# Performance work log

Measured on AMD Instinct MI355X. Metric: run time of the kernel, lower is better.

The kernel has to match this reference:

```python
import jax, jax.numpy as jnp
import numpy as np

EMBED = 1024
HEADS = 16
HEAD_DIM = EMBED // HEADS
SCALING = HEAD_DIM ** -0.5
R = 16
LORA_SCALE = 32.0 / R  # alpha / r
NEG = jnp.finfo(jnp.float32).min


def lora_linear(x, W, A, B):
    # y = x @ W.T + (x @ A.T) @ B.T * scale   (LinearLora, bias=False)
    return x @ W.T + ((x @ A.T) @ B.T) * LORA_SCALE


def setup_inputs() -> dict:
    key = jax.random.key(0)
    ks = jax.random.split(key, 14)
    B, T, D = 1, 4096, EMBED
    hidden_states = jax.random.normal(ks[0], (B, T, D), jnp.float32)
    # causal additive mask (bsz, 1, tgt, src): 0 on/below diag, dtype-min above
    i = jnp.arange(T)
    causal = jnp.where(i[:, None] >= i[None, :], 0.0, NEG).astype(jnp.float32)
    attention_mask = jnp.broadcast_to(causal, (B, 1, T, T))
    s = 0.02
    def w(k, shape):
        return jax.random.normal(k, shape, jnp.float32) * s
    return dict(
        hidden_states=hidden_states,
        attention_mask=attention_mask,
        Wq=w(ks[1], (D, D)), Wk=w(ks[2], (D, D)), Wv=w(ks[3], (D, D)), Wo=w(ks[4], (D, D)),
        Aq=w(ks[5], (R, D)), Bq=jnp.zeros((D, R), jnp.float32) + w(ks[6], (D, R)),
        Ak=w(ks[7], (R, D)), Bk=w(ks[8], (D, R)),
        Av=w(ks[9], (R, D)), Bv=w(ks[10], (D, R)),
        Ao=w(ks[11], (R, D)), Bo=w(ks[12], (D, R)),
    )


def reference(hidden_states, attention_mask, Wq, Wk, Wv, Wo,
              Aq, Bq, Ak, Bk, Av, Bv, Ao, Bo):
    bsz, tgt_len, _ = hidden_states.shape
    H, Hd = HEADS, HEAD_DIM

    q = lora_linear(hidden_states, Wq, Aq, Bq) * SCALING
    k = lora_linear(hidden_states, Wk, Ak, Bk)
    v = lora_linear(hidden_states, Wv, Av, Bv)

    # (b, t, H, Hd)
    q = q.reshape(bsz, tgt_len, H, Hd)
    k = k.reshape(bsz, tgt_len, H, Hd)
    v = v.reshape(bsz, tgt_len, H, Hd)

    # scores (b, H, t, s)
    attn = jnp.einsum('bthd,bshd->bhts', q, k)
    attn = attn + attention_mask
    attn = jnp.maximum(attn, NEG)
    attn = jax.nn.softmax(attn, axis=-1)  # dropout p=0 / eval mode

    out = jnp.einsum('bhts,bshd->bthd', attn, v)
    out = out.reshape(bsz, tgt_len, H * Hd)
    out = lora_linear(out, Wo, Ao, Bo)
    return out
```

## Files before the change

kernel.cpp:

```cpp
#include <hip/hip_runtime.h>
#include <cmath>
#include <cstdint>

typedef unsigned short u16;
typedef __attribute__((ext_vector_type(8))) __bf16 bf16x8;
typedef __attribute__((ext_vector_type(4))) __bf16 bf16x4;
typedef __attribute__((ext_vector_type(4))) short s16x4;
typedef __attribute__((ext_vector_type(4))) float f32x4;

__device__ __forceinline__ u16 f2bf(float f) {
    union { float f; unsigned u; } v; v.f = f;
    unsigned r = v.u + 0x7fffu + ((v.u >> 16) & 1u);
    return (u16)(r >> 16);
}

__device__ __forceinline__ void gload_lds(const u16* g, u16* l) {
    __builtin_amdgcn_global_load_lds((__attribute__((address_space(1))) void*)g,
                                     (__attribute__((address_space(3))) void*)l,
                                     16, 0, 0);
}

__device__ __forceinline__ f32x4 mfma16(s16x4 a, s16x4 b, f32x4 c) {
#if __has_builtin(__builtin_amdgcn_mfma_f32_16x16x16bf16_1k)
    return __builtin_amdgcn_mfma_f32_16x16x16bf16_1k(a, b, c, 0, 0, 0);
#else
    asm("v_mfma_f32_16x16x16_bf16 %0, %1, %2, %3"
        : "=v"(c) : "v"(a), "v"(b), "0"(c));
    return c;
#endif
}

__global__ __launch_bounds__(256) void prep_all(
        const float* __restrict__ X,
        const float* __restrict__ Wq, const float* __restrict__ Wk,
        const float* __restrict__ Wv, const float* __restrict__ Wo,
        const float* __restrict__ Aq, const float* __restrict__ Bq,
        const float* __restrict__ Ak, const float* __restrict__ Bk,
        const float* __restrict__ Av, const float* __restrict__ Bv,
        const float* __restrict__ Ao, const float* __restrict__ Bo,
        u16* __restrict__ Wqkv, u16* __restrict__ Wob, u16* __restrict__ Xb) {
    const int p = blockIdx.y;
    const int idx = blockIdx.x * 256 + threadIdx.x;
    if (p == 4) {
        float4 v = ((const float4*)X)[idx];
        ushort4 o;
        o.x = f2bf(v.x); o.y = f2bf(v.y); o.z = f2bf(v.z); o.w = f2bf(v.w);
        ((ushort4*)Xb)[idx] = o;
        return;
    }
    const int n = idx >> 10, d = idx & 1023;
    const float* W; const float* A; const float* B;
    switch (p) {
        case 0: W = Wq; A = Aq; B = Bq; break;
        case 1: W = Wk; A = Ak; B = Bk; break;
        case 2: W = Wv; A = Av; B = Bv; break;
        default: W = Wo; A = Ao; B = Bo; break;
    }
    float lora = 0.f;
#pragma unroll
    for (int r = 0; r < 16; r++) lora += B[n * 16 + r] * A[r * 1024 + d];
    float v = W[idx] + 2.0f * lora;
    if (p == 0) v *= 0.125f * 1.44269504088896340736f;
    if (p < 3) Wqkv[(size_t)p * 1048576 + idx] = f2bf(v);
    else       Wob[idx] = f2bf(v);
}

template <bool F32OUT>
__global__ __launch_bounds__(256, 3) void gemm_bt(const u16* __restrict__ A,
                                                  const u16* __restrict__ B,
                                                  void* __restrict__ C, int ldc) {
    __shared__ __align__(16) u16 As[128 * 64];
    __shared__ __align__(16) u16 Bs[128 * 64];
    const int tid = threadIdx.x;
    const int lane = tid & 63, wave = tid >> 6;
    const int quad = lane >> 4, l16 = lane & 15;
    const int wm = (wave >> 1) * 64, wn = (wave & 1) * 64;
    const size_t m0 = (size_t)blockIdx.y * 128, n0 = (size_t)blockIdx.x * 128;
    const u16* Ap = A + m0 * 1024;
    const u16* Bp = B + n0 * 1024;
    const int xsw = l16 & 7;
    f32x4 acc[4][4] = {};
    for (int k0 = 0; k0 < 1024; k0 += 64) {
#pragma unroll
        for (int hh = 0; hh < 4; hh++) {
            int c = tid + hh * 256;
            int row = c >> 3, cg = (c & 7) ^ (row & 7);
            gload_lds(Ap + (size_t)row * 1024 + k0 + cg * 8, As + c * 8);
            gload_lds(Bp + (size_t)row * 1024 + k0 + cg * 8, Bs + c * 8);
        }
        asm volatile("s_waitcnt vmcnt(0)" ::: "memory");
        __syncthreads();
#pragma unroll
        for (int kf = 0; kf < 2; kf++) {
            bf16x8 af[4], bfr[4];
#pragma unroll
            for (int i = 0; i < 4; i++) {
                af[i]  = *(const bf16x8*)(As + (wm + i * 16 + l16) * 64
                                             + ((kf * 4 + quad) ^ xsw) * 8);
                bfr[i] = *(const bf16x8*)(Bs + (wn + i * 16 + l16) * 64
                                             + ((kf * 4 + quad) ^ xsw) * 8);
            }
#pragma unroll
            for (int mi = 0; mi < 4; mi++)
#pragma unroll
                for (int ni = 0; ni < 4; ni++)
                    acc[mi][ni] = __builtin_amdgcn_mfma_f32_16x16x32_bf16(
                            af[mi], bfr[ni], acc[mi][ni], 0, 0, 0);
        }
        __syncthreads();
    }
#pragma unroll
    for (int mi = 0; mi < 4; mi++)
#pragma unroll
        for (int ni = 0; ni < 4; ni++)
#pragma unroll
            for (int r = 0; r < 4; r++) {
                size_t row = m0 + wm + mi * 16 + quad * 4 + r;
                size_t col = n0 + wn + ni * 16 + l16;
                if (F32OUT) ((float*)C)[row * ldc + col] = acc[mi][ni][r];
                else        ((u16*)C)[row * ldc + col] = f2bf(acc[mi][ni][r]);
            }
}

template <bool F32OUT>
__global__ __launch_bounds__(256, 3) void gemm_bt64(const u16* __restrict__ A,
                                                    const u16* __restrict__ B,
                                                    void* __restrict__ C, int ldc) {
    __shared__ __align__(16) u16 As[64 * 64];
    __shared__ __align__(16) u16 Bs[128 * 64];
    const int tid = threadIdx.x;
    const int lane = tid & 63, wave = tid >> 6;
    const int quad = lane >> 4, l16 = lane & 15;
    const int wm = (wave >> 1) * 32, wn = (wave & 1) * 64;
    const size_t m0 = (size_t)blockIdx.y * 64, n0 = (size_t)blockIdx.x * 128;
    const u16* Ap = A + m0 * 1024;
    const u16* Bp = B + n0 * 1024;
    const int xsw = l16 & 7;
    f32x4 acc[2][4] = {};
    for (int k0 = 0; k0 < 1024; k0 += 64) {
#pragma unroll
        for (int hh = 0; hh < 2; hh++) {
            int c = tid + hh * 256;
            int row = c >> 3, cg = (c & 7) ^ (row & 7);
            gload_lds(Ap + (size_t)row * 1024 + k0 + cg * 8, As + c * 8);
        }
#pragma unroll
        for (int hh = 0; hh < 4; hh++) {
            int c = tid + hh * 256;
            int row = c >> 3, cg = (c & 7) ^ (row & 7);
            gload_lds(Bp + (size_t)row * 1024 + k0 + cg * 8, Bs + c * 8);
        }
        asm volatile("s_waitcnt vmcnt(0)" ::: "memory");
        __syncthreads();
#pragma unroll
        for (int kf = 0; kf < 2; kf++) {
            bf16x8 af[2], bfr[4];
#pragma unroll
            for (int i = 0; i < 2; i++)
                af[i] = *(const bf16x8*)(As + (wm + i * 16 + l16) * 64
                                            + ((kf * 4 + quad) ^ xsw) * 8);
#pragma unroll
            for (int i = 0; i < 4; i++)
                bfr[i] = *(const bf16x8*)(Bs + (wn + i * 16 + l16) * 64
                                             + ((kf * 4 + quad) ^ xsw) * 8);
#pragma unroll
            for (int mi = 0; mi < 2; mi++)
#pragma unroll
                for (int ni = 0; ni < 4; ni++)
                    acc[mi][ni] = __builtin_amdgcn_mfma_f32_16x16x32_bf16(
                            af[mi], bfr[ni], acc[mi][ni], 0, 0, 0);
        }
        __syncthreads();
    }
#pragma unroll
    for (int mi = 0; mi < 2; mi++)
#pragma unroll
        for (int ni = 0; ni < 4; ni++)
#pragma unroll
            for (int r = 0; r < 4; r++) {
                size_t row = m0 + wm + mi * 16 + quad * 4 + r;
                size_t col = n0 + wn + ni * 16 + l16;
                if (F32OUT) ((float*)C)[row * ldc + col] = acc[mi][ni][r];
                else        ((u16*)C)[row * ldc + col] = f2bf(acc[mi][ni][r]);
            }
}

__global__ __launch_bounds__(256) void transpose_v(const u16* __restrict__ Y,
                                                   u16* __restrict__ Vt) {
    __shared__ u16 tile[64][68];
    const int dv0 = blockIdx.x * 64;
    const int t0  = blockIdx.y * 64;
    const int tid = threadIdx.x;
#pragma unroll
    for (int p = 0; p < 4; p++) {
        int pos = tid + p * 256;
        int row = pos >> 4;
        int c4  = (pos & 15) * 4;
        ushort4 v = *(const ushort4*)(Y + (size_t)(t0 + row) * 3072 + 2048 + dv0 + c4);
        tile[row][c4 + 0] = v.x; tile[row][c4 + 1] = v.y;
        tile[row][c4 + 2] = v.z; tile[row][c4 + 3] = v.w;
    }
    __syncthreads();
#pragma unroll
    for (int p = 0; p < 4; p++) {
        int pos = tid + p * 256;
        int orow = pos >> 4;
        int oc4  = (pos & 15) * 4;
        ushort4 o;
        o.x = tile[oc4 + 0][orow]; o.y = tile[oc4 + 1][orow];
        o.z = tile[oc4 + 2][orow]; o.w = tile[oc4 + 3][orow];
        *(ushort4*)(Vt + (size_t)(dv0 + orow) * 4096 + t0 + oc4) = o;
    }
}

__global__ __launch_bounds__(256, 4) void flash_attn(const u16* __restrict__ Y,
                                                     const u16* __restrict__ Vt,
                                                     u16* __restrict__ O) {
    __shared__ __align__(16) u16 lds[16384];
    const int tid = threadIdx.x;
    const int wave = tid >> 6, lane = tid & 63;
    const int quad = lane >> 4, l16 = lane & 15;
    const int bid = blockIdx.x;
    const int rr = bid & 255, j = bid >> 8;
    const int b = rr >> 4, h = rr & 15;
    int p;
    switch (j) { case 0:  p = 63 - b; break;
                 case 1:  p = 32 + b; break;
                 case 2:  p = 31 - b; break;
                 default: p = b;      break; }
    const int q0 = p * 64;
    const int q0w = q0 + wave * 16;
    const int nT = p + 1;
    const u16* Kbase = Y + 1024 + h * 64;
    const u16* Vbase = Vt + (size_t)(h * 64) * 4096;
    const int xsw = l16 & 7;

    bf16x8 qf[2];
#pragma unroll
    for (int kf = 0; kf < 2; kf++)
        qf[kf] = *(const bf16x8*)(Y + (size_t)(q0w + l16) * 3072
                                    + h * 64 + kf * 32 + quad * 8);

    f32x4 oaccT[4] = {};
    float l_i = 0.f;

#pragma unroll
    for (int pp = 0; pp < 2; pp++) {
        int c = pp * 256 + tid;
        int row = c >> 3, cg = (c & 7) ^ (row & 7);
        gload_lds(Kbase + (size_t)row * 3072 + cg * 8, lds + c * 8);
        gload_lds(Vbase + (size_t)row * 4096 + cg * 8, lds + 4096 + c * 8);
    }

#pragma unroll 1
    for (int t = 0; t < nT; t++) {
        const int s0 = t * 64;
        u16* Ks = lds + (t & 1) * 8192;
        u16* Vs = Ks + 4096;
        asm volatile("s_waitcnt vmcnt(0)" ::: "memory");
        __syncthreads();

        if (t + 1 < nT) {
            u16* Kn = lds + ((t + 1) & 1) * 8192;
            const int sn = s0 + 64;
#pragma unroll
            for (int pp = 0; pp < 2; pp++) {
                int c = pp * 256 + tid;
                int row = c >> 3, cg = (c & 7) ^ (row & 7);
                gload_lds(Kbase + (size_t)(sn + row) * 3072 + cg * 8, Kn + c * 8);
                gload_lds(Vbase + (size_t)row * 4096 + sn + cg * 8, Kn + 4096 + c * 8);
            }
        }

        bf16x8 kfr[4][2];
#pragma unroll
        for (int ni = 0; ni < 4; ni++) {
            int row = ni * 16 + l16;
            kfr[ni][0] = *(const bf16x8*)(Ks + row * 64 + ((quad) ^ xsw) * 8);
            kfr[ni][1] = *(const bf16x8*)(Ks + row * 64 + ((4 + quad) ^ xsw) * 8);
        }
        s16x4 vfr[4][4];
#pragma unroll
        for (int nj = 0; nj < 4; nj++) {
            int row = nj * 16 + l16;
#pragma unroll
            for (int ni = 0; ni < 4; ni++) {
                int cc = ni * 2 + (quad >> 1);
                vfr[nj][ni] = *(const s16x4*)(Vs + row * 64 + (cc ^ xsw) * 8
                                                 + (quad & 1) * 4);
            }
        }
        asm volatile("s_waitcnt lgkmcnt(0)" ::: "memory");

        f32x4 sacc[4] = {};
#pragma unroll
        for (int ni = 0; ni < 4; ni++) {
            sacc[ni] = __builtin_amdgcn_mfma_f32_16x16x32_bf16(
                    kfr[ni][0], qf[0], sacc[ni], 0, 0, 0);
            sacc[ni] = __builtin_amdgcn_mfma_f32_16x16x32_bf16(
                    kfr[ni][1], qf[1], sacc[ni], 0, 0, 0);
        }

        if (t == nT - 1) {
            const int qg = q0w + l16;
#pragma unroll
            for (int ni = 0; ni < 4; ni++)
#pragma unroll
                for (int r = 0; r < 4; r++) {
                    int sg = s0 + ni * 16 + quad * 4 + r;
                    if (sg > qg) sacc[ni][r] = -INFINITY;
                }
        }
        float rs = 0.f;
        s16x4 pf[4];
#pragma unroll
        for (int ni = 0; ni < 4; ni++) {
            f32x4 pe;
#pragma unroll
            for (int r = 0; r < 4; r++) {
                pe[r] = __builtin_amdgcn_exp2f(sacc[ni][r]);
                rs += pe[r];
            }
            bf16x4 tt = { (__bf16)pe[0], (__bf16)pe[1],
                          (__bf16)pe[2], (__bf16)pe[3] };
            pf[ni] = __builtin_bit_cast(s16x4, tt);
        }
        rs += __shfl_xor(rs, 16);
        rs += __shfl_xor(rs, 32);
        l_i += rs;

#pragma unroll
        for (int nj = 0; nj < 4; nj++)
#pragma unroll
            for (int ni = 0; ni < 4; ni++)
                oaccT[nj] = mfma16(vfr[nj][ni], pf[ni], oaccT[nj]);
    }

    __syncthreads();
    u16* scr = lds + wave * 1152;
    {
        float inv = 1.0f / l_i;
#pragma unroll
        for (int nj = 0; nj < 4; nj++) {
            bf16x4 t4 = { (__bf16)(oaccT[nj][0] * inv),
                          (__bf16)(oaccT[nj][1] * inv),
                          (__bf16)(oaccT[nj][2] * inv),
                          (__bf16)(oaccT[nj][3] * inv) };
            *(s16x4*)(scr + l16 * 72 + nj * 16 + quad * 4) =
                    __builtin_bit_cast(s16x4, t4);
        }
    }
    asm volatile("s_waitcnt lgkmcnt(0)" ::: "memory");
#pragma unroll
    for (int pp = 0; pp < 2; pp++) {
        int row = pp * 8 + (lane >> 3);
        int seg = (lane & 7) * 8;
        bf16x8 d = *(const bf16x8*)(scr + row * 72 + seg);
        *(bf16x8*)(O + (size_t)(q0w + row) * 1024 + h * 64 + seg) = d;
    }
}


extern "C" void kernel_launch(void* const* d_in, const int* in_sizes, int n_in,
                              void* d_out, int out_size, void* d_ws, size_t ws_size,
                              hipStream_t stream) {
    const float* X  = (const float*)d_in[0];
    const float* Wq = (const float*)d_in[2];
    const float* Wk = (const float*)d_in[3];
    const float* Wv = (const float*)d_in[4];
    const float* Wo = (const float*)d_in[5];
    const float* Aq = (const float*)d_in[6];
    const float* Bq = (const float*)d_in[7];
    const float* Ak = (const float*)d_in[8];
    const float* Bk = (const float*)d_in[9];
    const float* Av = (const float*)d_in[10];
    const float* Bv = (const float*)d_in[11];
    const float* Ao = (const float*)d_in[12];
    const float* Bo = (const float*)d_in[13];

    char* ws = (char*)d_ws;
    u16* Xb   = (u16*)(ws);
    u16* Wqkv = (u16*)(ws + (8u  << 20));
    u16* Wob  = (u16*)(ws + (14u << 20));
    u16* Y    = (u16*)(ws + (16u << 20));
    u16* Vt   = (u16*)(ws + (40u << 20));
    u16* Ob   = (u16*)(ws + (48u << 20));

    prep_all<<<dim3(4096, 5), 256, 0, stream>>>(X, Wq, Wk, Wv, Wo, Aq, Bq, Ak, Bk,
                                                Av, Bv, Ao, Bo, Wqkv, Wob, Xb);
    gemm_bt<false><<<dim3(24, 32), 256, 0, stream>>>(Xb, Wqkv, Y, 3072);
    transpose_v<<<dim3(16, 64), 256, 0, stream>>>(Y, Vt);
    flash_attn<<<dim3(1024), 256, 0, stream>>>(Y, Vt, Ob);
    gemm_bt64<true><<<dim3(8, 64), 256, 0, stream>>>(Ob, Wob, d_out, 1024);
}
```

Measured before the change: 257.3 us.

## Fuse V transpose into QKV GEMM epilogue and widen flash-attention query tiles

```diff
diff --git a/kernel.cpp b/kernel.cpp
--- a/kernel.cpp
+++ b/kernel.cpp
@@ -65,10 +65,10 @@
     else       Wob[idx] = f2bf(v);
 }
 
-template <bool F32OUT>
-__global__ __launch_bounds__(256, 3) void gemm_bt(const u16* __restrict__ A,
-                                                  const u16* __restrict__ B,
-                                                  void* __restrict__ C, int ldc) {
+__global__ __launch_bounds__(256, 3) void gemm_qkv(const u16* __restrict__ A,
+                                                   const u16* __restrict__ B,
+                                                   u16* __restrict__ Y,
+                                                   u16* __restrict__ Vt) {
     __shared__ __align__(16) u16 As[128 * 64];
     __shared__ __align__(16) u16 Bs[128 * 64];
     const int tid = threadIdx.x;
@@ -109,23 +109,35 @@
         }
         __syncthreads();
     }
-#pragma unroll
-    for (int mi = 0; mi < 4; mi++)
-#pragma unroll
-        for (int ni = 0; ni < 4; ni++)
-#pragma unroll
-            for (int r = 0; r < 4; r++) {
-                size_t row = m0 + wm + mi * 16 + quad * 4 + r;
-                size_t col = n0 + wn + ni * 16 + l16;
-                if (F32OUT) ((float*)C)[row * ldc + col] = acc[mi][ni][r];
-                else        ((u16*)C)[row * ldc + col] = f2bf(acc[mi][ni][r]);
-            }
-}
-
-template <bool F32OUT>
+    if (n0 >= 2048) {
+#pragma unroll
+        for (int mi = 0; mi < 4; mi++)
+#pragma unroll
+            for (int ni = 0; ni < 4; ni++) {
+                size_t dv = n0 - 2048 + wn + ni * 16 + l16;
+                size_t t  = m0 + wm + mi * 16 + quad * 4;
+                ushort4 pk;
+                pk.x = f2bf(acc[mi][ni][0]); pk.y = f2bf(acc[mi][ni][1]);
+                pk.z = f2bf(acc[mi][ni][2]); pk.w = f2bf(acc[mi][ni][3]);
+                *(ushort4*)(Vt + dv * 4096 + t) = pk;
+            }
+    } else {
+#pragma unroll
+        for (int mi = 0; mi < 4; mi++)
+#pragma unroll
+            for (int ni = 0; ni < 4; ni++)
+#pragma unroll
+                for (int r = 0; r < 4; r++) {
+                    size_t row = m0 + wm + mi * 16 + quad * 4 + r;
+                    size_t col = n0 + wn + ni * 16 + l16;
+                    Y[row * 2048 + col] = f2bf(acc[mi][ni][r]);
+                }
+    }
+}
+
 __global__ __launch_bounds__(256, 3) void gemm_bt64(const u16* __restrict__ A,
                                                     const u16* __restrict__ B,
-                                                    void* __restrict__ C, int ldc) {
+                                                    float* __restrict__ C) {
     __shared__ __align__(16) u16 As[64 * 64];
     __shared__ __align__(16) u16 Bs[128 * 64];
     const int tid = threadIdx.x;
@@ -180,75 +192,43 @@
             for (int r = 0; r < 4; r++) {
                 size_t row = m0 + wm + mi * 16 + quad * 4 + r;
                 size_t col = n0 + wn + ni * 16 + l16;
-                if (F32OUT) ((float*)C)[row * ldc + col] = acc[mi][ni][r];
-                else        ((u16*)C)[row * ldc + col] = f2bf(acc[mi][ni][r]);
-            }
-}
-
-__global__ __launch_bounds__(256) void transpose_v(const u16* __restrict__ Y,
-                                                   u16* __restrict__ Vt) {
-    __shared__ u16 tile[64][68];
-    const int dv0 = blockIdx.x * 64;
-    const int t0  = blockIdx.y * 64;
-    const int tid = threadIdx.x;
-#pragma unroll
-    for (int p = 0; p < 4; p++) {
-        int pos = tid + p * 256;
-        int row = pos >> 4;
-        int c4  = (pos & 15) * 4;
-        ushort4 v = *(const ushort4*)(Y + (size_t)(t0 + row) * 3072 + 2048 + dv0 + c4);
-        tile[row][c4 + 0] = v.x; tile[row][c4 + 1] = v.y;
-        tile[row][c4 + 2] = v.z; tile[row][c4 + 3] = v.w;
-    }
-    __syncthreads();
-#pragma unroll
-    for (int p = 0; p < 4; p++) {
-        int pos = tid + p * 256;
-        int orow = pos >> 4;
-        int oc4  = (pos & 15) * 4;
-        ushort4 o;
-        o.x = tile[oc4 + 0][orow]; o.y = tile[oc4 + 1][orow];
-        o.z = tile[oc4 + 2][orow]; o.w = tile[oc4 + 3][orow];
-        *(ushort4*)(Vt + (size_t)(dv0 + orow) * 4096 + t0 + oc4) = o;
-    }
-}
-
-__global__ __launch_bounds__(256, 4) void flash_attn(const u16* __restrict__ Y,
+                C[row * 1024 + col] = acc[mi][ni][r];
+            }
+}
+
+__global__ __launch_bounds__(256, 2) void flash_attn(const u16* __restrict__ Y,
                                                      const u16* __restrict__ Vt,
                                                      u16* __restrict__ O) {
     __shared__ __align__(16) u16 lds[16384];
     const int tid = threadIdx.x;
     const int wave = tid >> 6, lane = tid & 63;
     const int quad = lane >> 4, l16 = lane & 15;
-    const int bid = blockIdx.x;
-    const int rr = bid & 255, j = bid >> 8;
-    const int b = rr >> 4, h = rr & 15;
-    int p;
-    switch (j) { case 0:  p = 63 - b; break;
-                 case 1:  p = 32 + b; break;
-                 case 2:  p = 31 - b; break;
-                 default: p = b;      break; }
-    const int q0 = p * 64;
-    const int q0w = q0 + wave * 16;
-    const int nT = p + 1;
+    const int idx = blockIdx.x;
+    int h, qb;
+    if (idx < 256) { h = idx & 15; qb = 31 - (idx >> 4); }
+    else           { h = (idx - 256) & 15; qb = (idx - 256) >> 4; }
+    const int q0w = qb * 128 + wave * 32;
+    const int nT = 2 * qb + 2;
     const u16* Kbase = Y + 1024 + h * 64;
     const u16* Vbase = Vt + (size_t)(h * 64) * 4096;
     const int xsw = l16 & 7;
 
-    bf16x8 qf[2];
-#pragma unroll
-    for (int kf = 0; kf < 2; kf++)
-        qf[kf] = *(const bf16x8*)(Y + (size_t)(q0w + l16) * 3072
-                                    + h * 64 + kf * 32 + quad * 8);
-
-    f32x4 oaccT[4] = {};
-    float l_i = 0.f;
+    bf16x8 qf[2][2];
+#pragma unroll
+    for (int mi = 0; mi < 2; mi++)
+#pragma unroll
+        for (int kf = 0; kf < 2; kf++)
+            qf[mi][kf] = *(const bf16x8*)(Y + (size_t)(q0w + mi * 16 + l16) * 2048
+                                            + h * 64 + kf * 32 + quad * 8);
+
+    f32x4 oaccT[2][4] = {};
+    float l_i[2] = {0.f, 0.f};
 
 #pragma unroll
     for (int pp = 0; pp < 2; pp++) {
         int c = pp * 256 + tid;
         int row = c >> 3, cg = (c & 7) ^ (row & 7);
-        gload_lds(Kbase + (size_t)row * 3072 + cg * 8, lds + c * 8);
+        gload_lds(Kbase + (size_t)row * 2048 + cg * 8, lds + c * 8);
         gload_lds(Vbase + (size_t)row * 4096 + cg * 8, lds + 4096 + c * 8);
     }
 
@@ -267,92 +247,103 @@
             for (int pp = 0; pp < 2; pp++) {
                 int c = pp * 256 + tid;
                 int row = c >> 3, cg = (c & 7) ^ (row & 7);
-                gload_lds(Kbase + (size_t)(sn + row) * 3072 + cg * 8, Kn + c * 8);
+                gload_lds(Kbase + (size_t)(sn + row) * 2048 + cg * 8, Kn + c * 8);
                 gload_lds(Vbase + (size_t)row * 4096 + sn + cg * 8, Kn + 4096 + c * 8);
             }
         }
 
-        bf16x8 kfr[4][2];
-#pragma unroll
-        for (int ni = 0; ni < 4; ni++) {
-            int row = ni * 16 + l16;
-            kfr[ni][0] = *(const bf16x8*)(Ks + row * 64 + ((quad) ^ xsw) * 8);
-            kfr[ni][1] = *(const bf16x8*)(Ks + row * 64 + ((4 + quad) ^ xsw) * 8);
-        }
-        s16x4 vfr[4][4];
+        if (s0 <= q0w + 31) {
+            bf16x8 kfr[4][2];
+#pragma unroll
+            for (int ni = 0; ni < 4; ni++) {
+                int row = ni * 16 + l16;
+                kfr[ni][0] = *(const bf16x8*)(Ks + row * 64 + ((quad) ^ xsw) * 8);
+                kfr[ni][1] = *(const bf16x8*)(Ks + row * 64 + ((4 + quad) ^ xsw) * 8);
+            }
+            s16x4 vfr[4][4];
+#pragma unroll
+            for (int nj = 0; nj < 4; nj++) {
+                int row = nj * 16 + l16;
+#pragma unroll
+                for (int ni = 0; ni < 4; ni++) {
+                    int cc = ni * 2 + (quad >> 1);
+                    vfr[nj][ni] = *(const s16x4*)(Vs + row * 64 + (cc ^ xsw) * 8
+                                                     + (quad & 1) * 4);
+                }
+            }
+            asm volatile("s_waitcnt lgkmcnt(0)" ::: "memory");
+
+            f32x4 sacc[2][4] = {};
+#pragma unroll
+            for (int mi = 0; mi < 2; mi++)
+#pragma unroll
+                for (int ni = 0; ni < 4; ni++) {
+                    sacc[mi][ni] = __builtin_amdgcn_mfma_f32_16x16x32_bf16(
+                            kfr[ni][0], qf[mi][0], sacc[mi][ni], 0, 0, 0);
+                    sacc[mi][ni] = __builtin_amdgcn_mfma_f32_16x16x32_bf16(
+                            kfr[ni][1], qf[mi][1], sacc[mi][ni], 0, 0, 0);
+                }
+
+            const bool maskit = (s0 + 63 > q0w);
+            s16x4 pf[2][4];
+#pragma unroll
+            for (int mi = 0; mi < 2; mi++) {
+                if (maskit) {
+                    const int qg = q0w + mi * 16 + l16;
+#pragma unroll
+                    for (int ni = 0; ni < 4; ni++)
+#pragma unroll
+                        for (int r = 0; r < 4; r++) {
+                            int sg = s0 + ni * 16 + quad * 4 + r;
+                            if (sg > qg) sacc[mi][ni][r] = -INFINITY;
+                        }
+                }
+                float rs = 0.f;
+#pragma unroll
+                for (int ni = 0; ni < 4; ni++) {
+                    f32x4 pe;
+#pragma unroll
+                    for (int r = 0; r < 4; r++) {
+                        pe[r] = __builtin_amdgcn_exp2f(sacc[mi][ni][r]);
+                        rs += pe[r];
+                    }
+                    bf16x4 tt = { (__bf16)pe[0], (__bf16)pe[1],
+                                  (__bf16)pe[2], (__bf16)pe[3] };
+                    pf[mi][ni] = __builtin_bit_cast(s16x4, tt);
+                }
+                rs += __shfl_xor(rs, 16);
+                rs += __shfl_xor(rs, 32);
+                l_i[mi] += rs;
+            }
+
+#pragma unroll
+            for (int nj = 0; nj < 4; nj++)
+#pragma unroll
+                for (int ni = 0; ni < 4; ni++) {
+                    oaccT[0][nj] = mfma16(vfr[nj][ni], pf[0][ni], oaccT[0][nj]);
+                    oaccT[1][nj] = mfma16(vfr[nj][ni], pf[1][ni], oaccT[1][nj]);
+                }
+        }
+    }
+
+    __syncthreads();
+    u16* scr = lds + wave * 2304;
+#pragma unroll
+    for (int mi = 0; mi < 2; mi++) {
+        float inv = 1.0f / l_i[mi];
 #pragma unroll
         for (int nj = 0; nj < 4; nj++) {
-            int row = nj * 16 + l16;
-#pragma unroll
-            for (int ni = 0; ni < 4; ni++) {
-                int cc = ni * 2 + (quad >> 1);
-                vfr[nj][ni] = *(const s16x4*)(Vs + row * 64 + (cc ^ xsw) * 8
-                                                 + (quad & 1) * 4);
-            }
-        }
-        asm volatile("s_waitcnt lgkmcnt(0)" ::: "memory");
-
-        f32x4 sacc[4] = {};
-#pragma unroll
-        for (int ni = 0; ni < 4; ni++) {
-            sacc[ni] = __builtin_amdgcn_mfma_f32_16x16x32_bf16(
-                    kfr[ni][0], qf[0], sacc[ni], 0, 0, 0);
-            sacc[ni] = __builtin_amdgcn_mfma_f32_16x16x32_bf16(
-                    kfr[ni][1], qf[1], sacc[ni], 0, 0, 0);
-        }
-
-        if (t == nT - 1) {
-            const int qg = q0w + l16;
-#pragma unroll
-            for (int ni = 0; ni < 4; ni++)
-#pragma unroll
-                for (int r = 0; r < 4; r++) {
-                    int sg = s0 + ni * 16 + quad * 4 + r;
-                    if (sg > qg) sacc[ni][r] = -INFINITY;
-                }
-        }
-        float rs = 0.f;
-        s16x4 pf[4];
-#pragma unroll
-        for (int ni = 0; ni < 4; ni++) {
-            f32x4 pe;
-#pragma unroll
-            for (int r = 0; r < 4; r++) {
-                pe[r] = __builtin_amdgcn_exp2f(sacc[ni][r]);
-                rs += pe[r];
-            }
-            bf16x4 tt = { (__bf16)pe[0], (__bf16)pe[1],
-                          (__bf16)pe[2], (__bf16)pe[3] };
-            pf[ni] = __builtin_bit_cast(s16x4, tt);
-        }
-        rs += __shfl_xor(rs, 16);
-        rs += __shfl_xor(rs, 32);
-        l_i += rs;
-
-#pragma unroll
-        for (int nj = 0; nj < 4; nj++)
-#pragma unroll
-            for (int ni = 0; ni < 4; ni++)
-                oaccT[nj] = mfma16(vfr[nj][ni], pf[ni], oaccT[nj]);
-    }
-
-    __syncthreads();
-    u16* scr = lds + wave * 1152;
-    {
-        float inv = 1.0f / l_i;
-#pragma unroll
-        for (int nj = 0; nj < 4; nj++) {
-            bf16x4 t4 = { (__bf16)(oaccT[nj][0] * inv),
-                          (__bf16)(oaccT[nj][1] * inv),
-                          (__bf16)(oaccT[nj][2] * inv),
-                          (__bf16)(oaccT[nj][3] * inv) };
-            *(s16x4*)(scr + l16 * 72 + nj * 16 + quad * 4) =
+            bf16x4 t4 = { (__bf16)(oaccT[mi][nj][0] * inv),
+                          (__bf16)(oaccT[mi][nj][1] * inv),
+                          (__bf16)(oaccT[mi][nj][2] * inv),
+                          (__bf16)(oaccT[mi][nj][3] * inv) };
+            *(s16x4*)(scr + (mi * 16 + l16) * 72 + nj * 16 + quad * 4) =
                     __builtin_bit_cast(s16x4, t4);
         }
     }
     asm volatile("s_waitcnt lgkmcnt(0)" ::: "memory");
 #pragma unroll
-    for (int pp = 0; pp < 2; pp++) {
+    for (int pp = 0; pp < 4; pp++) {
         int row = pp * 8 + (lane >> 3);
         int seg = (lane & 7) * 8;
         bf16x8 d = *(const bf16x8*)(scr + row * 72 + seg);
@@ -383,13 +374,12 @@
     u16* Wqkv = (u16*)(ws + (8u  << 20));
     u16* Wob  = (u16*)(ws + (14u << 20));
     u16* Y    = (u16*)(ws + (16u << 20));
-    u16* Vt   = (u16*)(ws + (40u << 20));
-    u16* Ob   = (u16*)(ws + (48u << 20));
+    u16* Vt   = (u16*)(ws + (32u << 20));
+    u16* Ob   = (u16*)(ws + (40u << 20));
 
     prep_all<<<dim3(4096, 5), 256, 0, stream>>>(X, Wq, Wk, Wv, Wo, Aq, Bq, Ak, Bk,
                                                 Av, Bv, Ao, Bo, Wqkv, Wob, Xb);
-    gemm_bt<false><<<dim3(24, 32), 256, 0, stream>>>(Xb, Wqkv, Y, 3072);
-    transpose_v<<<dim3(16, 64), 256, 0, stream>>>(Y, Vt);
-    flash_attn<<<dim3(1024), 256, 0, stream>>>(Y, Vt, Ob);
-    gemm_bt64<true><<<dim3(8, 64), 256, 0, stream>>>(Ob, Wob, d_out, 1024);
-}
+    gemm_qkv<<<dim3(24, 32), 256, 0, stream>>>(Xb, Wqkv, Y, Vt);
+    flash_attn<<<dim3(512), 256, 0, stream>>>(Y, Vt, Ob);
+    gemm_bt64<<<dim3(8, 64), 256, 0, stream>>>(Ob, Wob, (float*)d_out);
+}
```

Result: slower. 275.8 us (+7.2%).

## Fuse V transpose into QKV GEMM epilogue and double-buffer GEMM K loops

Applied to the files above, without the earlier changes.

```diff
diff --git a/kernel.cpp b/kernel.cpp
--- a/kernel.cpp
+++ b/kernel.cpp
@@ -65,12 +65,11 @@
     else       Wob[idx] = f2bf(v);
 }
 
-template <bool F32OUT>
-__global__ __launch_bounds__(256, 3) void gemm_bt(const u16* __restrict__ A,
-                                                  const u16* __restrict__ B,
-                                                  void* __restrict__ C, int ldc) {
-    __shared__ __align__(16) u16 As[128 * 64];
-    __shared__ __align__(16) u16 Bs[128 * 64];
+__global__ __launch_bounds__(256, 3) void gemm_qkv(const u16* __restrict__ A,
+                                                   const u16* __restrict__ B,
+                                                   u16* __restrict__ Y,
+                                                   u16* __restrict__ Vt) {
+    __shared__ __align__(16) u16 sh[16384];
     const int tid = threadIdx.x;
     const int lane = tid & 63, wave = tid >> 6;
     const int quad = lane >> 4, l16 = lane & 15;
@@ -78,56 +77,97 @@
     const size_t m0 = (size_t)blockIdx.y * 128, n0 = (size_t)blockIdx.x * 128;
     const u16* Ap = A + m0 * 1024;
     const u16* Bp = B + n0 * 1024;
-    const int xsw = l16 & 7;
+    const int xsw = l16 & 3;
     f32x4 acc[4][4] = {};
-    for (int k0 = 0; k0 < 1024; k0 += 64) {
-#pragma unroll
-        for (int hh = 0; hh < 4; hh++) {
-            int c = tid + hh * 256;
-            int row = c >> 3, cg = (c & 7) ^ (row & 7);
-            gload_lds(Ap + (size_t)row * 1024 + k0 + cg * 8, As + c * 8);
-            gload_lds(Bp + (size_t)row * 1024 + k0 + cg * 8, Bs + c * 8);
-        }
+
+#pragma unroll
+    for (int hh = 0; hh < 2; hh++) {
+        int c = tid + hh * 256;
+        int row = c >> 2, cg = (c & 3) ^ (row & 3);
+        gload_lds(Ap + (size_t)row * 1024 + cg * 8, sh + c * 8);
+        gload_lds(Bp + (size_t)row * 1024 + cg * 8, sh + 8192 + c * 8);
+    }
+
+#pragma unroll 1
+    for (int t = 0; t < 32; t++) {
+        const u16* Asc = sh + (t & 1) * 4096;
+        const u16* Bsc = sh + 8192 + (t & 1) * 4096;
         asm volatile("s_waitcnt vmcnt(0)" ::: "memory");
         __syncthreads();
-#pragma unroll
-        for (int kf = 0; kf < 2; kf++) {
-            bf16x8 af[4], bfr[4];
-#pragma unroll
-            for (int i = 0; i < 4; i++) {
-                af[i]  = *(const bf16x8*)(As + (wm + i * 16 + l16) * 64
-                                             + ((kf * 4 + quad) ^ xsw) * 8);
-                bfr[i] = *(const bf16x8*)(Bs + (wn + i * 16 + l16) * 64
-                                             + ((kf * 4 + quad) ^ xsw) * 8);
-            }
-#pragma unroll
-            for (int mi = 0; mi < 4; mi++)
-#pragma unroll
-                for (int ni = 0; ni < 4; ni++)
-                    acc[mi][ni] = __builtin_amdgcn_mfma_f32_16x16x32_bf16(
-                            af[mi], bfr[ni], acc[mi][ni], 0, 0, 0);
-        }
+        if (t + 1 < 32) {
+            const int k1 = (t + 1) * 32;
+            u16* An = sh + ((t + 1) & 1) * 4096;
+            u16* Bn = sh + 8192 + ((t + 1) & 1) * 4096;
+#pragma unroll
+            for (int hh = 0; hh < 2; hh++) {
+                int c = tid + hh * 256;
+                int row = c >> 2, cg = (c & 3) ^ (row & 3);
+                gload_lds(Ap + (size_t)row * 1024 + k1 + cg * 8, An + c * 8);
+                gload_lds(Bp + (size_t)row * 1024 + k1 + cg * 8, Bn + c * 8);
+            }
+        }
+        bf16x8 af[4], bfr[4];
+#pragma unroll
+        for (int i = 0; i < 4; i++) {
+            af[i]  = *(const bf16x8*)(Asc + (wm + i * 16 + l16) * 32
+                                          + (quad ^ xsw) * 8);
+            bfr[i] = *(const bf16x8*)(Bsc + (wn + i * 16 + l16) * 32
+                                          + (quad ^ xsw) * 8);
+        }
+#pragma unroll
+        for (int mi = 0; mi < 4; mi++)
+#pragma unroll
+            for (int ni = 0; ni < 4; ni++)
+                acc[mi][ni] = __builtin_amdgcn_mfma_f32_16x16x32_bf16(
+                        af[mi], bfr[ni], acc[mi][ni], 0, 0, 0);
+    }
+
+    if (n0 >= 2048) {
         __syncthreads();
-    }
-#pragma unroll
-    for (int mi = 0; mi < 4; mi++)
-#pragma unroll
-        for (int ni = 0; ni < 4; ni++)
-#pragma unroll
-            for (int r = 0; r < 4; r++) {
-                size_t row = m0 + wm + mi * 16 + quad * 4 + r;
-                size_t col = n0 + wn + ni * 16 + l16;
-                if (F32OUT) ((float*)C)[row * ldc + col] = acc[mi][ni][r];
-                else        ((u16*)C)[row * ldc + col] = f2bf(acc[mi][ni][r]);
-            }
-}
-
-template <bool F32OUT>
+        u16* scr = sh + wave * 2176;
+#pragma unroll 1
+        for (int ps = 0; ps < 2; ps++) {
+#pragma unroll
+            for (int nn = 0; nn < 2; nn++) {
+                int ni = ps * 2 + nn;
+#pragma unroll
+                for (int mi = 0; mi < 4; mi++) {
+                    ushort4 pk;
+                    pk.x = f2bf(acc[mi][ni][0]); pk.y = f2bf(acc[mi][ni][1]);
+                    pk.z = f2bf(acc[mi][ni][2]); pk.w = f2bf(acc[mi][ni][3]);
+                    *(ushort4*)(scr + (nn * 16 + l16) * 68 + mi * 16 + quad * 4) = pk;
+                }
+            }
+            asm volatile("s_waitcnt lgkmcnt(0)" ::: "memory");
+#pragma unroll
+            for (int pp = 0; pp < 4; pp++) {
+                int row = pp * 8 + (lane >> 3);
+                int ck  = (lane & 7) * 8;
+                bf16x8 d = *(const bf16x8*)(scr + row * 68 + ck);
+                size_t dv = n0 - 2048 + wn + ps * 32 + row;
+                *(bf16x8*)(Vt + dv * 4096 + m0 + wm + ck) = d;
+            }
+            asm volatile("s_waitcnt lgkmcnt(0)" ::: "memory");
+        }
+    } else {
+#pragma unroll
+        for (int mi = 0; mi < 4; mi++)
+#pragma unroll
+            for (int ni = 0; ni < 4; ni++)
+#pragma unroll
+                for (int r = 0; r < 4; r++) {
+                    size_t row = m0 + wm + mi * 16 + quad * 4 + r;
+                    size_t col = n0 + wn + ni * 16 + l16;
+                    Y[row * 2048 + col] = f2bf(acc[mi][ni][r]);
+                }
+    }
+}
+
 __global__ __launch_bounds__(256, 3) void gemm_bt64(const u16* __restrict__ A,
                                                     const u16* __restrict__ B,
-                                                    void* __restrict__ C, int ldc) {
-    __shared__ __align__(16) u16 As[64 * 64];
-    __shared__ __align__(16) u16 Bs[128 * 64];
+                                                    float* __restrict__ C) {
+    __shared__ __align__(16) u16 As[2][64 * 32];
+    __shared__ __align__(16) u16 Bs[2][128 * 32];
     const int tid = threadIdx.x;
     const int lane = tid & 63, wave = tid >> 6;
     const int quad = lane >> 4, l16 = lane & 15;
@@ -135,42 +175,53 @@
     const size_t m0 = (size_t)blockIdx.y * 64, n0 = (size_t)blockIdx.x * 128;
     const u16* Ap = A + m0 * 1024;
     const u16* Bp = B + n0 * 1024;
-    const int xsw = l16 & 7;
+    const int xsw = l16 & 3;
     f32x4 acc[2][4] = {};
-    for (int k0 = 0; k0 < 1024; k0 += 64) {
+
+    {
+        int c = tid;
+        int row = c >> 2, cg = (c & 3) ^ (row & 3);
+        gload_lds(Ap + (size_t)row * 1024 + cg * 8, As[0] + c * 8);
 #pragma unroll
         for (int hh = 0; hh < 2; hh++) {
-            int c = tid + hh * 256;
-            int row = c >> 3, cg = (c & 7) ^ (row & 7);
-            gload_lds(Ap + (size_t)row * 1024 + k0 + cg * 8, As + c * 8);
-        }
-#pragma unroll
-        for (int hh = 0; hh < 4; hh++) {
-            int c = tid + hh * 256;
-            int row = c >> 3, cg = (c & 7) ^ (row & 7);
-            gload_lds(Bp + (size_t)row * 1024 + k0 + cg * 8, Bs + c * 8);
-        }
+            int b = tid + hh * 256;
+            int brow = b >> 2, bcg = (b & 3) ^ (brow & 3);
+            gload_lds(Bp + (size_t)brow * 1024 + bcg * 8, Bs[0] + b * 8);
+        }
+    }
+
+#pragma unroll 1
+    for (int t = 0; t < 32; t++) {
+        const int cb = t & 1;
         asm volatile("s_waitcnt vmcnt(0)" ::: "memory");
         __syncthreads();
-#pragma unroll
-        for (int kf = 0; kf < 2; kf++) {
-            bf16x8 af[2], bfr[4];
-#pragma unroll
-            for (int i = 0; i < 2; i++)
-                af[i] = *(const bf16x8*)(As + (wm + i * 16 + l16) * 64
-                                            + ((kf * 4 + quad) ^ xsw) * 8);
-#pragma unroll
-            for (int i = 0; i < 4; i++)
-                bfr[i] = *(const bf16x8*)(Bs + (wn + i * 16 + l16) * 64
-                                             + ((kf * 4 + quad) ^ xsw) * 8);
-#pragma unroll
-            for (int mi = 0; mi < 2; mi++)
-#pragma unroll
-                for (int ni = 0; ni < 4; ni++)
-                    acc[mi][ni] = __builtin_amdgcn_mfma_f32_16x16x32_bf16(
-                            af[mi], bfr[ni], acc[mi][ni], 0, 0, 0);
-        }
-        __syncthreads();
+        if (t + 1 < 32) {
+            const int k1 = (t + 1) * 32, nb = cb ^ 1;
+            int c = tid;
+            int row = c >> 2, cg = (c & 3) ^ (row & 3);
+            gload_lds(Ap + (size_t)row * 1024 + k1 + cg * 8, As[nb] + c * 8);
+#pragma unroll
+            for (int hh = 0; hh < 2; hh++) {
+                int b = tid + hh * 256;
+                int brow = b >> 2, bcg = (b & 3) ^ (brow & 3);
+                gload_lds(Bp + (size_t)brow * 1024 + k1 + bcg * 8, Bs[nb] + b * 8);
+            }
+        }
+        bf16x8 af[2], bfr[4];
+#pragma unroll
+        for (int i = 0; i < 2; i++)
+            af[i] = *(const bf16x8*)(As[cb] + (wm + i * 16 + l16) * 32
+                                            + (quad ^ xsw) * 8);
+#pragma unroll
+        for (int i = 0; i < 4; i++)
+            bfr[i] = *(const bf16x8*)(Bs[cb] + (wn + i * 16 + l16) * 32
+                                             + (quad ^ xsw) * 8);
+#pragma unroll
+        for (int mi = 0; mi < 2; mi++)
+#pragma unroll
+            for (int ni = 0; ni < 4; ni++)
+                acc[mi][ni] = __builtin_amdgcn_mfma_f32_16x16x32_bf16(
+                        af[mi], bfr[ni], acc[mi][ni], 0, 0, 0);
     }
 #pragma unroll
     for (int mi = 0; mi < 2; mi++)
@@ -180,37 +231,8 @@
             for (int r = 0; r < 4; r++) {
                 size_t row = m0 + wm + mi * 16 + quad * 4 + r;
                 size_t col = n0 + wn + ni * 16 + l16;
-                if (F32OUT) ((float*)C)[row * ldc + col] = acc[mi][ni][r];
-                else        ((u16*)C)[row * ldc + col] = f2bf(acc[mi][ni][r]);
-            }
-}
-
-__global__ __launch_bounds__(256) void transpose_v(const u16* __restrict__ Y,
-                                                   u16* __restrict__ Vt) {
-    __shared__ u16 tile[64][68];
-    const int dv0 = blockIdx.x * 64;
-    const int t0  = blockIdx.y * 64;
-    const int tid = threadIdx.x;
-#pragma unroll
-    for (int p = 0; p < 4; p++) {
-        int pos = tid + p * 256;
-        int row = pos >> 4;
-        int c4  = (pos & 15) * 4;
-        ushort4 v = *(const ushort4*)(Y + (size_t)(t0 + row) * 3072 + 2048 + dv0 + c4);
-        tile[row][c4 + 0] = v.x; tile[row][c4 + 1] = v.y;
-        tile[row][c4 + 2] = v.z; tile[row][c4 + 3] = v.w;
-    }
-    __syncthreads();
-#pragma unroll
-    for (int p = 0; p < 4; p++) {
-        int pos = tid + p * 256;
-        int orow = pos >> 4;
-        int oc4  = (pos & 15) * 4;
-        ushort4 o;
-        o.x = tile[oc4 + 0][orow]; o.y = tile[oc4 + 1][orow];
-        o.z = tile[oc4 + 2][orow]; o.w = tile[oc4 + 3][orow];
-        *(ushort4*)(Vt + (size_t)(dv0 + orow) * 4096 + t0 + oc4) = o;
-    }
+                C[row * 1024 + col] = acc[mi][ni][r];
+            }
 }
 
 __global__ __launch_bounds__(256, 4) void flash_attn(const u16* __restrict__ Y,
@@ -228,8 +250,7 @@
                  case 1:  p = 32 + b; break;
                  case 2:  p = 31 - b; break;
                  default: p = b;      break; }
-    const int q0 = p * 64;
-    const int q0w = q0 + wave * 16;
+    const int q0w = p * 64 + wave * 16;
     const int nT = p + 1;
     const u16* Kbase = Y + 1024 + h * 64;
     const u16* Vbase = Vt + (size_t)(h * 64) * 4096;
@@ -238,7 +259,7 @@
     bf16x8 qf[2];
 #pragma unroll
     for (int kf = 0; kf < 2; kf++)
-        qf[kf] = *(const bf16x8*)(Y + (size_t)(q0w + l16) * 3072
+        qf[kf] = *(const bf16x8*)(Y + (size_t)(q0w + l16) * 2048
                                     + h * 64 + kf * 32 + quad * 8);
 
     f32x4 oaccT[4] = {};
@@ -248,7 +269,7 @@
     for (int pp = 0; pp < 2; pp++) {
         int c = pp * 256 + tid;
         int row = c >> 3, cg = (c & 7) ^ (row & 7);
-        gload_lds(Kbase + (size_t)row * 3072 + cg * 8, lds + c * 8);
+        gload_lds(Kbase + (size_t)row * 2048 + cg * 8, lds + c * 8);
         gload_lds(Vbase + (size_t)row * 4096 + cg * 8, lds + 4096 + c * 8);
     }
 
@@ -267,7 +288,7 @@
             for (int pp = 0; pp < 2; pp++) {
                 int c = pp * 256 + tid;
                 int row = c >> 3, cg = (c & 7) ^ (row & 7);
-                gload_lds(Kbase + (size_t)(sn + row) * 3072 + cg * 8, Kn + c * 8);
+                gload_lds(Kbase + (size_t)(sn + row) * 2048 + cg * 8, Kn + c * 8);
                 gload_lds(Vbase + (size_t)row * 4096 + sn + cg * 8, Kn + 4096 + c * 8);
             }
         }
@@ -383,13 +404,12 @@
     u16* Wqkv = (u16*)(ws + (8u  << 20));
     u16* Wob  = (u16*)(ws + (14u << 20));
     u16* Y    = (u16*)(ws + (16u << 20));
-    u16* Vt   = (u16*)(ws + (40u << 20));
-    u16* Ob   = (u16*)(ws + (48u << 20));
+    u16* Vt   = (u16*)(ws + (32u << 20));
+    u16* Ob   = (u16*)(ws + (40u << 20));
 
     prep_all<<<dim3(4096, 5), 256, 0, stream>>>(X, Wq, Wk, Wv, Wo, Aq, Bq, Ak, Bk,
                                                 Av, Bv, Ao, Bo, Wqkv, Wob, Xb);
-    gemm_bt<false><<<dim3(24, 32), 256, 0, stream>>>(Xb, Wqkv, Y, 3072);
-    transpose_v<<<dim3(16, 64), 256, 0, stream>>>(Y, Vt);
+    gemm_qkv<<<dim3(24, 32), 256, 0, stream>>>(Xb, Wqkv, Y, Vt);
     flash_attn<<<dim3(1024), 256, 0, stream>>>(Y, Vt, Ob);
-    gemm_bt64<true><<<dim3(8, 64), 256, 0, stream>>>(Ob, Wob, d_out, 1024);
-}
+    gemm_bt64<<<dim3(8, 64), 256, 0, stream>>>(Ob, Wob, (float*)d_out);
+}
```

Result: slower. 680.5 us (+164.5%).
